# Kernel tuning notes

Measured on AMD Instinct MI355X. Metric: run time of the kernel, lower is better.

## Reference

```python
import jax, jax.numpy as jnp
import numpy as np

N_NODES = 100_000
N_EDGES = 1_000_000
IN_CH = 32
EDGE_CH = 16
OUT_CH = 32
D_CAT = 2 * IN_CH + EDGE_CH  # 80
D_MID = 56                   # linspace(80, 32, 3)[1]


def setup_inputs() -> dict:
    key = jax.random.key(0)
    ks = jax.random.split(key, 8)
    x = jax.random.normal(ks[0], (N_NODES, IN_CH), dtype=jnp.float32)
    edge_index = jax.random.randint(ks[1], (2, N_EDGES), 0, N_NODES, dtype=jnp.int64)
    edge_attr = jax.random.normal(ks[2], (N_EDGES, EDGE_CH), dtype=jnp.float32)
    # MLP params: Linear(80->56), Linear(56->32), bias=True (homogeneous_flag=False)
    W1 = jax.random.normal(ks[3], (D_CAT, D_MID), dtype=jnp.float32) / np.sqrt(D_CAT).astype(np.float32)
    b1 = jnp.zeros((D_MID,), dtype=jnp.float32)
    W2 = jax.random.normal(ks[4], (D_MID, OUT_CH), dtype=jnp.float32) / np.sqrt(D_MID).astype(np.float32)
    b2 = jnp.zeros((OUT_CH,), dtype=jnp.float32)
    return {"x": x, "edge_index": edge_index, "edge_attr": edge_attr,
            "W1": W1, "b1": b1, "W2": W2, "b2": b2}


def reference(x, edge_index, edge_attr, W1, b1, W2, b2):
    num_nodes = x.shape[0]
    rol, col = edge_index[0], edge_index[1]
    # gather node pairs + concat edge features: [E, 2*in + edge]
    e = jnp.concatenate([x[rol], x[col], edge_attr], axis=-1)
    # edge MLP (LeakyReLU after every layer, as in IterGNN's MLP)
    h = jax.nn.leaky_relu(e @ W1 + b1)
    v = jax.nn.leaky_relu(h @ W2 + b2)  # [E, out]
    # Max aggregation by destination node (scatter-max); empty segments -> 0
    agg = jax.ops.segment_max(v, col, num_segments=num_nodes)
    agg = jnp.where(jnp.isneginf(agg), jnp.zeros((), dtype=agg.dtype), agg)
    # elementwise max with trailing slice of input features
    out = jnp.maximum(agg, x[:, -v.shape[-1]:])
    return out
```

## Files before the change

### kernel.cpp

```cpp
#include <hip/hip_runtime.h>

#define N_NODES 100000
#define IN_CH 32
#define EDGE_CH 16
#define OUT_CH 32
#define D_CAT 80
#define D_MID 56

#define BKT_SHIFT 6
#define BKT_NODES 64
#define NB 1563
#define NB_ALL 1568
#define CAP 1024

#define NSUP 196
#define CAP_SUP 5632
#define K1_EDGES 4096
#define K2_ITERS 11

#define EPB 256
#define NT_E 16

#define W1F_SH 4096
#define W2F_SH 2048
#define W1D_SH 2048
#define WIMG_SH (W1F_SH + W2F_SH + W1D_SH)
#define FEATF_SH (NT_E * 2 * 64 * 8)

#define HSTRIDE 68
#define AGG_LD 33
#define ENC_NEGINF 0x007FFFFFu

typedef short short8 __attribute__((ext_vector_type(8)));
typedef float f32x4 __attribute__((ext_vector_type(4)));
typedef int i32x2 __attribute__((ext_vector_type(2)));

#define WS_IMG    0
#define WS_B1     16384
#define WS_B2     16640
#define WS_SUPCNT 16768
#define WS_GCNT   17664
#define WS_SUPREC 24576
#define WS_REC    8855552
#define WS_XB_A   21700608
#define XB_BYTES  6400000
#define WS_NEED_A ((size_t)WS_XB_A)
#define WS_NEED_AX ((size_t)WS_XB_A + XB_BYTES)
#define WS_XB_B   12869632
#define WS_NEED_B ((size_t)WS_XB_B)
#define WS_NEED_BX ((size_t)WS_XB_B + XB_BYTES)

__device__ __forceinline__ unsigned fenc(float f) {
    unsigned u = __float_as_uint(f);
    return (u & 0x80000000u) ? ~u : (u | 0x80000000u);
}
__device__ __forceinline__ float fdec(unsigned u) {
    u = (u & 0x80000000u) ? (u ^ 0x80000000u) : ~u;
    return __uint_as_float(u);
}
__device__ __forceinline__ float bfr(float f) {
    unsigned u = __float_as_uint(f);
    u = (u + 0x7FFFu + ((u >> 16) & 1u)) & 0xFFFF0000u;
    return __uint_as_float(u);
}
__device__ __forceinline__ unsigned short bf16b(float f) {
    unsigned u = __float_as_uint(f);
    return (unsigned short)((u + 0x7FFFu + ((u >> 16) & 1u)) >> 16);
}
__device__ __forceinline__ short8 cvt8(float4 a, float4 b) {
    return short8{ (short)bf16b(a.x), (short)bf16b(a.y), (short)bf16b(a.z), (short)bf16b(a.w),
                   (short)bf16b(b.x), (short)bf16b(b.y), (short)bf16b(b.z), (short)bf16b(b.w) };
}

__device__ __forceinline__ void convert_x_bf16(const float* __restrict__ x,
                                               unsigned short* __restrict__ xb,
                                               int gtid, int gstride) {
    const int tot = N_NODES * IN_CH / 8;
    for (int i = gtid; i < tot; i += gstride) {
        float4 a = ((const float4*)x)[2 * i];
        float4 b = ((const float4*)x)[2 * i + 1];
        *(short8*)&xb[i * 8] = cvt8(a, b);
    }
}

__device__ void build_weight_image(const float* __restrict__ W1, const float* __restrict__ b1,
                                   const float* __restrict__ W2, const float* __restrict__ b2,
                                   unsigned short* __restrict__ wsImg,
                                   float* __restrict__ wsb1, float* __restrict__ wsb2,
                                   int t, int nthr) {
    for (int s = t; s < W1F_SH; s += nthr) {
        int j = s & 7, l = (s >> 3) & 63, fi = s >> 9;
        int nt = fi & 3, ks = fi >> 2;
        int n = nt * 16 + (l & 15), kl = ks * 32 + (l >> 4) * 8 + j;
        unsigned short v = 0;
        if (n < D_MID) {
            if (kl < 32) v = bf16b(W1[kl * D_MID + n]);
            else if (kl < 48) v = bf16b(W1[(64 + kl - 32) * D_MID + n]);
        }
        wsImg[s] = v;
    }
    for (int s = t; s < W2F_SH; s += nthr) {
        int j = s & 7, l = (s >> 3) & 63, fi = s >> 9;
        int nt = fi & 1, ks = fi >> 1;
        int n = nt * 16 + (l & 15), kl = ks * 32 + (l >> 4) * 8 + j;
        wsImg[W1F_SH + s] = (kl < D_MID) ? bf16b(W2[kl * OUT_CH + n]) : (unsigned short)0;
    }
    for (int s = t; s < W1D_SH; s += nthr) {
        int j = s & 7, l = (s >> 3) & 63, fi = s >> 9;
        int nt = fi & 3;
        int n = nt * 16 + (l & 15), kl = (l >> 4) * 8 + j;
        wsImg[W1F_SH + W2F_SH + s] = (n < D_MID) ? bf16b(W1[(32 + kl) * D_MID + n]) : (unsigned short)0;
    }
    if (t < 64) wsb1[t] = (t < D_MID) ? bfr(b1[t]) : 0.f;
    else if (t < 96) wsb2[t - 64] = bfr(b2[t - 64]);
}

__global__ __launch_bounds__(512) void coarse_bin(
    const int* __restrict__ ei, int nE, int* __restrict__ gSupCnt, int2* __restrict__ supRec,
    const float* __restrict__ W1, const float* __restrict__ b1,
    const float* __restrict__ W2, const float* __restrict__ b2,
    unsigned short* __restrict__ wsImg, float* __restrict__ wsb1, float* __restrict__ wsb2)
{
    __shared__ int2 staged[K1_EDGES];
    __shared__ int cnt[256], sc[256], cur[256], wb[256];
    const int t = threadIdx.x;
    if (blockIdx.x == 0) build_weight_image(W1, b1, W2, b2, wsImg, wsb1, wsb2, t, 512);
    if (t < 256) cnt[t] = 0;
    __syncthreads();

    const int lo = blockIdx.x * K1_EDGES;
    int rdst[8], rsrc[8];
#pragma unroll
    for (int k = 0; k < 8; ++k) {
        int e = lo + k * 512 + t;
        bool v = e < nE;
        rdst[k] = v ? __builtin_nontemporal_load(ei + nE + e) : -1;
        rsrc[k] = v ? __builtin_nontemporal_load(ei + e) : 0;
        if ((unsigned)rdst[k] >= N_NODES) rdst[k] = -1;
        if ((unsigned)rsrc[k] >= N_NODES) rsrc[k] = 0;
        if (rdst[k] >= 0) atomicAdd(&cnt[rdst[k] >> 9], 1);
    }
    __syncthreads();
    if (t < 256) sc[t] = cnt[t];
    __syncthreads();
    for (int off = 1; off < 256; off <<= 1) {
        int v = 0;
        if (t < 256 && t >= off) v = sc[t - off];
        __syncthreads();
        if (t < 256) sc[t] += v;
        __syncthreads();
    }
    if (t < NSUP) {
        int c = cnt[t];
        int excl = sc[t] - c;
        int g = c ? atomicAdd(&gSupCnt[t], c) : 0;
        wb[t] = t * CAP_SUP + g - excl;
        cur[t] = excl;
    }
    __syncthreads();
#pragma unroll
    for (int k = 0; k < 8; ++k) {
        if (rdst[k] >= 0) {
            int s = rdst[k] >> 9;
            int pos = atomicAdd(&cur[s], 1);
            int e = lo + k * 512 + t;
            staged[pos] = make_int2(rsrc[k] | (s << 24), ((rdst[k] & 511) << 20) | e);
        }
    }
    __syncthreads();
    int nv = sc[NSUP - 1];
    for (int i = t; i < nv; i += 512) {
        int2 r = staged[i];
        int s = (unsigned)r.x >> 24;
        int addr = wb[s] + i;
        if (addr - s * CAP_SUP < CAP_SUP)
            supRec[addr] = make_int2(r.x & 0x00FFFFFF, r.y);
    }
}

__global__ __launch_bounds__(512) void fine_bin(
    const int* __restrict__ gSupCnt, const int2* __restrict__ supRec,
    int* __restrict__ gCnt, int2* __restrict__ rec,
    const float* __restrict__ x, unsigned short* __restrict__ xb)
{
    __shared__ int cur8[8];
    const int s = blockIdx.x, t = threadIdx.x;
    const int lane = t & 63;

    if (xb) convert_x_bf16(x, xb, s * 512 + t, NSUP * 512);

    const int cntS = min(gSupCnt[s], CAP_SUP);
    if (t < 8) cur8[t] = 0;
    __syncthreads();

    int2 r[K2_ITERS];
#pragma unroll
    for (int k = 0; k < K2_ITERS; ++k) {
        int i = k * 512 + t;
        r[k] = (i < cntS) ? supRec[(size_t)s * CAP_SUP + i] : make_int2(0, 0);
    }
#pragma unroll
    for (int k = 0; k < K2_ITERS; ++k) {
        int i = k * 512 + t;
        bool v = i < cntS;
        int f = v ? ((r[k].y >> 26) & 7) : -1;
        int rank = 0, wbase = 0;
#pragma unroll
        for (int vv = 0; vv < 8; ++vv) {
            unsigned long long m = __ballot(f == vv);
            if (lane == vv) wbase = m ? atomicAdd(&cur8[vv], (int)__popcll(m)) : 0;
            if (f == vv) rank = (int)__popcll(m & ((1ull << lane) - 1ull));
        }
        int base = __shfl(wbase, f & 7);
        if (v) {
            int pos = base + rank;
            if (pos < CAP)
                rec[(size_t)(s * 8 + f) * CAP + pos] =
                    make_int2(r[k].x, (((r[k].y >> 20) & 63) << 20) | (r[k].y & 0xFFFFF));
        }
    }
    __syncthreads();
    if (t < 8) gCnt[s * 8 + t] = min(cur8[t], CAP);
}

__global__ __launch_bounds__(512) void scatter_append(
    const int* __restrict__ ei, int* __restrict__ gCnt, int2* __restrict__ rec, int nE,
    const float* __restrict__ W1, const float* __restrict__ b1,
    const float* __restrict__ W2, const float* __restrict__ b2,
    unsigned short* __restrict__ wsImg, float* __restrict__ wsb1, float* __restrict__ wsb2,
    const float* __restrict__ x, unsigned short* __restrict__ xb)
{
    __shared__ int lh[NB];
    __shared__ int lbase[NB];
    if (blockIdx.x == 0) build_weight_image(W1, b1, W2, b2, wsImg, wsb1, wsb2, threadIdx.x, 512);
    if (xb) convert_x_bf16(x, xb, blockIdx.x * 512 + threadIdx.x, gridDim.x * 512);
    for (int i = threadIdx.x; i < NB; i += 512) lh[i] = 0;
    __syncthreads();
    int per = (nE + gridDim.x - 1) / gridDim.x;
    int lo = blockIdx.x * per;
    int hi = min(lo + per, nE);
    for (int e = lo + threadIdx.x; e < hi; e += 512) {
        int dst = __builtin_nontemporal_load(ei + nE + e);
        if ((unsigned)dst < N_NODES) atomicAdd(&lh[dst >> BKT_SHIFT], 1);
    }
    __syncthreads();
    for (int i = threadIdx.x; i < NB; i += 512) {
        int c = lh[i];
        lbase[i] = c ? atomicAdd(&gCnt[i], c) : 0;
        lh[i] = 0;
    }
    __syncthreads();
    for (int e = lo + threadIdx.x; e < hi; e += 512) {
        int dst = __builtin_nontemporal_load(ei + nE + e);
        if ((unsigned)dst >= N_NODES) continue;
        int b = dst >> BKT_SHIFT;
        int p = lbase[b] + atomicAdd(&lh[b], 1);
        if (p >= CAP) continue;
        int src = __builtin_nontemporal_load(ei + e);
        if ((unsigned)src >= N_NODES) src = 0;
        rec[(size_t)b * CAP + p] = make_int2(src, ((dst & (BKT_NODES - 1)) << 20) | e);
    }
}

template<int XB>
__global__ __launch_bounds__(512, 4) void bucket_mlp(
    const float* __restrict__ x, const unsigned short* __restrict__ xb,
    const float* __restrict__ ea,
    const int2* __restrict__ rec, const int* __restrict__ gCnt,
    const unsigned short* __restrict__ wsImg,
    const float* __restrict__ wsb1, const float* __restrict__ wsb2,
    float* __restrict__ out)
{
    __shared__ unsigned short sFeatF[FEATF_SH];
    __shared__ unsigned short sWgt[WIMG_SH];
    __shared__ float sHdst[BKT_NODES * HSTRIDE];
    __shared__ unsigned aggL[BKT_NODES * AGG_LD];
    __shared__ float sb1f[64];
    __shared__ float sb2f[32];
    __shared__ int sdl[EPB];

    unsigned short* const sW1F = sWgt;
    unsigned short* const sW2F = sWgt + W1F_SH;
    unsigned short* const sW1D = sWgt + W1F_SH + W2F_SH;
    unsigned short* const sHF  = sFeatF;

    const int t = threadIdx.x;
    const int nodeBase = blockIdx.x << BKT_SHIFT;
    const int base = blockIdx.x * CAP;
    const int cnt  = min(gCnt[blockIdx.x], CAP);

    for (int i = t; i < WIMG_SH / 8; i += 512)
        *(short8*)&sWgt[i * 8] = *(const short8*)(wsImg + i * 8);
    for (int i = t; i < BKT_NODES * AGG_LD; i += 512) aggL[i] = ENC_NEGINF;
    if (t < 64) sb1f[t] = wsb1[t];
    else if (t < 96) sb2f[t - 64] = wsb2[t - 64];

    const int wave = t >> 6;
    const int l15  = t & 15;
    const int quad = (t & 63) >> 4;
    const int lane = t & 63;
    const int slot = t >> 1, q = t & 1;
    const int sl15 = slot & 15, set = slot >> 4;

    short8 rv16[4];
    int rdl;

    auto loadRec = [&](int idx) -> i32x2 {
        return (idx < cnt) ? *(const i32x2*)(rec + base + idx) : (i32x2){0, 0};
    };
    auto gather = [&](i32x2 r2, bool ok) {
        rdl = ok ? ((r2.y >> 20) & 63) : -1;
        short8 z = {0, 0, 0, 0, 0, 0, 0, 0};
        if (q == 0) {
            if constexpr (XB) {
                const short8* xs8 = (const short8*)(xb + (size_t)r2.x * IN_CH);
#pragma unroll
                for (int k = 0; k < 4; ++k) rv16[k] = ok ? xs8[k] : z;
            } else {
                const float* xs = x + (size_t)r2.x * IN_CH;
#pragma unroll
                for (int k = 0; k < 4; ++k)
                    rv16[k] = ok ? cvt8(((const float4*)xs)[2 * k], ((const float4*)xs)[2 * k + 1]) : z;
            }
        } else {
            const float* ep = ea + (size_t)(r2.y & 0xFFFFF) * EDGE_CH;
#pragma unroll
            for (int k = 0; k < 2; ++k)
                rv16[k] = ok ? cvt8(((const float4*)ep)[2 * k], ((const float4*)ep)[2 * k + 1]) : z;
            rv16[2] = z; rv16[3] = z;
        }
    };
    auto storeChunk = [&]() {
        if (q == 0) sdl[slot] = rdl;
#pragma unroll
        for (int k = 0; k < 4; ++k) {
            int cj = q * 4 + k;
            int a16 = (set * 2 + (cj >> 2)) * 64 + (cj & 3) * 16 + sl15;
            *(short8*)&sFeatF[a16 * 8] = rv16[k];
        }
    };

    i32x2 recC = loadRec(slot);
    i32x2 recN = loadRec(EPB + slot);
    gather(recC, slot < cnt);

    __syncthreads();

    {
        const int ntile = wave & 3, mh = wave >> 2;
        int node = nodeBase + ntile * 16 + l15;
        short8 bfr8 = {0, 0, 0, 0, 0, 0, 0, 0};
        if (node < N_NODES) {
            if constexpr (XB) {
                bfr8 = *(const short8*)(xb + (size_t)node * IN_CH + quad * 8);
            } else {
                const float* xp = x + (size_t)node * IN_CH + quad * 8;
                bfr8 = cvt8(((const float4*)xp)[0], ((const float4*)xp)[1]);
            }
        }
        f32x4 accd[2] = {(f32x4){0.f, 0.f, 0.f, 0.f}, (f32x4){0.f, 0.f, 0.f, 0.f}};
#pragma unroll
        for (int i = 0; i < 2; ++i) {
            int nt = mh * 2 + i;
            short8 af = *(const short8*)&sW1D[(nt * 64 + lane) * 8];
            accd[i] = __builtin_amdgcn_mfma_f32_16x16x32_bf16(af, bfr8, accd[i], 0, 0, 0);
        }
#pragma unroll
        for (int i = 0; i < 2; ++i) {
            int nt = mh * 2 + i, c0 = nt * 16 + quad * 4;
            float4 vv;
#pragma unroll
            for (int j = 0; j < 4; ++j) {
                int c = c0 + j;
                ((float*)&vv)[j] = (c < D_MID) ? accd[i][j] + sb1f[c] : 0.f;
            }
            *(float4*)&sHdst[(ntile * 16 + l15) * HSTRIDE + c0] = vv;
        }
    }

    for (int c0e = 0; c0e < cnt; c0e += EPB) {
        storeChunk();
        __syncthreads();
        gather(recN, (c0e + EPB + slot) < cnt);
        recN = loadRec(c0e + 2 * EPB + slot);

        f32x4 acc[2][4];
#pragma unroll
        for (int ei = 0; ei < 2; ++ei)
#pragma unroll
            for (int nt = 0; nt < 4; ++nt) acc[ei][nt] = (f32x4){0.f, 0.f, 0.f, 0.f};
#pragma unroll
        for (int ks = 0; ks < 2; ++ks) {
            short8 bf0 = *(const short8*)&sFeatF[((wave * 2 + ks) * 64 + lane) * 8];
            short8 bf1 = *(const short8*)&sFeatF[(((wave + 8) * 2 + ks) * 64 + lane) * 8];
#pragma unroll
            for (int nt = 0; nt < 4; ++nt) {
                short8 af = *(const short8*)&sW1F[((ks * 4 + nt) * 64 + lane) * 8];
                acc[0][nt] = __builtin_amdgcn_mfma_f32_16x16x32_bf16(af, bf0, acc[0][nt], 0, 0, 0);
                acc[1][nt] = __builtin_amdgcn_mfma_f32_16x16x32_bf16(af, bf1, acc[1][nt], 0, 0, 0);
            }
        }
        __syncthreads();

#pragma unroll
        for (int ei = 0; ei < 2; ++ei) {
            int et = wave + ei * 8;
            int dl = sdl[et * 16 + l15];
            const float* hrow = &sHdst[((dl >= 0) ? dl : 0) * HSTRIDE];
#pragma unroll
            for (int nt = 0; nt < 4; ++nt) {
                int c0 = nt * 16 + quad * 4;
                float4 hd = *(const float4*)&hrow[c0];
                int ks2 = nt >> 1;
                int quad2 = (nt * 2 + (quad >> 1)) & 3;
                int off = (quad & 1) * 4;
                ushort4 p;
#pragma unroll
                for (int j = 0; j < 4; ++j) {
                    float v = acc[ei][nt][j] + ((const float*)&hd)[j];
                    v = (v > 0.f) ? v : 0.01f * v;
                    ((unsigned short*)&p)[j] = (c0 + j < D_MID) ? bf16b(v) : (unsigned short)0;
                }
                *(ushort4*)&sHF[((et * 2 + ks2) * 64 + quad2 * 16 + l15) * 8 + off] = p;
            }
        }
        __syncthreads();

        f32x4 acc2[2][2];
#pragma unroll
        for (int ei = 0; ei < 2; ++ei)
#pragma unroll
            for (int nt = 0; nt < 2; ++nt) acc2[ei][nt] = (f32x4){0.f, 0.f, 0.f, 0.f};
#pragma unroll
        for (int ks = 0; ks < 2; ++ks) {
            short8 bf0 = *(const short8*)&sHF[((wave * 2 + ks) * 64 + lane) * 8];
            short8 bf1 = *(const short8*)&sHF[(((wave + 8) * 2 + ks) * 64 + lane) * 8];
#pragma unroll
            for (int nt = 0; nt < 2; ++nt) {
                short8 af = *(const short8*)&sW2F[((ks * 2 + nt) * 64 + lane) * 8];
                acc2[0][nt] = __builtin_amdgcn_mfma_f32_16x16x32_bf16(af, bf0, acc2[0][nt], 0, 0, 0);
                acc2[1][nt] = __builtin_amdgcn_mfma_f32_16x16x32_bf16(af, bf1, acc2[1][nt], 0, 0, 0);
            }
        }

#pragma unroll
        for (int ei = 0; ei < 2; ++ei) {
            int et = wave + ei * 8;
            int dl = sdl[et * 16 + l15];
            if (dl >= 0) {
                unsigned* arow = &aggL[dl * AGG_LD];
#pragma unroll
                for (int nt = 0; nt < 2; ++nt) {
                    int c0 = nt * 16 + quad * 4;
#pragma unroll
                    for (int j = 0; j < 4; ++j) {
                        float v = acc2[ei][nt][j] + sb2f[c0 + j];
                        v = (v > 0.f) ? v : 0.01f * v;
                        atomicMax(arow + c0 + j, fenc(bfr(v)));
                    }
                }
            }
        }
        __syncthreads();
    }
    __syncthreads();

    {
        int nl = t >> 3, g4 = t & 7;
        int node = nodeBase + nl;
        if (node < N_NODES) {
            const unsigned* ar = &aggL[nl * AGG_LD + g4 * 4];
            float4 o;
            if constexpr (XB) {
                ushort4 xw = ((const ushort4*)(xb + (size_t)node * IN_CH))[g4];
                o.x = fmaxf((ar[0] == ENC_NEGINF) ? 0.f : fdec(ar[0]), __uint_as_float((unsigned)xw.x << 16));
                o.y = fmaxf((ar[1] == ENC_NEGINF) ? 0.f : fdec(ar[1]), __uint_as_float((unsigned)xw.y << 16));
                o.z = fmaxf((ar[2] == ENC_NEGINF) ? 0.f : fdec(ar[2]), __uint_as_float((unsigned)xw.z << 16));
                o.w = fmaxf((ar[3] == ENC_NEGINF) ? 0.f : fdec(ar[3]), __uint_as_float((unsigned)xw.w << 16));
            } else {
                float4 xv = ((const float4*)(x + (size_t)node * IN_CH))[g4];
                o.x = fmaxf((ar[0] == ENC_NEGINF) ? 0.f : fdec(ar[0]), bfr(xv.x));
                o.y = fmaxf((ar[1] == ENC_NEGINF) ? 0.f : fdec(ar[1]), bfr(xv.y));
                o.z = fmaxf((ar[2] == ENC_NEGINF) ? 0.f : fdec(ar[2]), bfr(xv.z));
                o.w = fmaxf((ar[3] == ENC_NEGINF) ? 0.f : fdec(ar[3]), bfr(xv.w));
            }
            ((float4*)(out + (size_t)node * OUT_CH))[g4] = o;
        }
    }
}

extern "C" void kernel_launch(void* const* d_in, const int* in_sizes, int n_in,
                              void* d_out, int out_size, void* d_ws, size_t ws_size,
                              hipStream_t stream) {
    const float* x  = (const float*)d_in[0];
    const int*   ei = (const int*)d_in[1];
    const float* ea = (const float*)d_in[2];
    const float* W1 = (const float*)d_in[3];
    const float* b1 = (const float*)d_in[4];
    const float* W2 = (const float*)d_in[5];
    const float* b2 = (const float*)d_in[6];

    char* ws = (char*)d_ws;
    unsigned short* wsImg = (unsigned short*)(ws + WS_IMG);
    float* wsb1 = (float*)(ws + WS_B1);
    float* wsb2 = (float*)(ws + WS_B2);
    int* gSupCnt = (int*)(ws + WS_SUPCNT);
    int* gCnt = (int*)(ws + WS_GCNT);

    const int nE = in_sizes[1] / 2;
    float* out = (float*)d_out;

    if (ws_size >= WS_NEED_A) {
        int2* supRec = (int2*)(ws + WS_SUPREC);
        int2* rec    = (int2*)(ws + WS_REC);
        bool xbOn = ws_size >= WS_NEED_AX;
        unsigned short* xb = xbOn ? (unsigned short*)(ws + WS_XB_A) : nullptr;
        hipMemsetAsync(gSupCnt, 0, NSUP * sizeof(int), stream);
        coarse_bin<<<(nE + K1_EDGES - 1) / K1_EDGES, 512, 0, stream>>>(
            ei, nE, gSupCnt, supRec, W1, b1, W2, b2, wsImg, wsb1, wsb2);
        fine_bin<<<NSUP, 512, 0, stream>>>(gSupCnt, supRec, gCnt, rec, x, xb);
        if (xbOn)
            bucket_mlp<1><<<NB, 512, 0, stream>>>(x, xb, ea, rec, gCnt, wsImg, wsb1, wsb2, out);
        else
            bucket_mlp<0><<<NB, 512, 0, stream>>>(x, nullptr, ea, rec, gCnt, wsImg, wsb1, wsb2, out);
    } else {
        int2* rec = (int2*)(ws + 24576);
        bool xbOn = ws_size >= WS_NEED_BX;
        unsigned short* xb = xbOn ? (unsigned short*)(ws + WS_XB_B) : nullptr;
        hipMemsetAsync(gCnt, 0, NB_ALL * sizeof(int), stream);
        scatter_append<<<128, 512, 0, stream>>>(ei, gCnt, rec, nE, W1, b1, W2, b2,
                                                wsImg, wsb1, wsb2, x, xb);
        if (xbOn)
            bucket_mlp<1><<<NB, 512, 0, stream>>>(x, xb, ea, rec, gCnt, wsImg, wsb1, wsb2, out);
        else
            bucket_mlp<0><<<NB, 512, 0, stream>>>(x, nullptr, ea, rec, gCnt, wsImg, wsb1, wsb2, out);
    }
}
```

Before: 208.5 us.

## Simplify coarse binning and split fine binning across blocks with global atomics

The coarse binning kernel drops its LDS staging buffer and block-wide prefix scan. Each edge record is now written straight to its super-bucket slot, using a global atomic base plus a local counter, and each block handles half as many edges. The fine binning kernel splits every super-bucket across four blocks that reserve bucket slots with global atomics on gCnt, which is now zeroed by a widened memset. The aim is more parallelism and fewer barriers in the preprocessing stages, at the cost of scattered uncoalesced writes, more global atomic traffic and gCnt no longer being clamped to CAP.

```diff
diff --git a/kernel.cpp b/kernel.cpp
--- a/kernel.cpp
+++ b/kernel.cpp
@@ -15,8 +15,11 @@
 
 #define NSUP 196
 #define CAP_SUP 5632
-#define K1_EDGES 4096
-#define K2_ITERS 11
+#define K1_EDGES 2048
+#define K1_EPT 4
+#define K2_SPLIT 4
+#define K2_SLICE 1408
+#define K2_SITERS 3
 
 #define EPB 256
 #define NT_E 16
@@ -40,6 +43,8 @@
 #define WS_B2     16640
 #define WS_SUPCNT 16768
 #define WS_GCNT   17664
+#define WS_Z0     16768
+#define WS_ZSZ    (17664 + 6272 - 16768)
 #define WS_SUPREC 24576
 #define WS_REC    8855552
 #define WS_XB_A   21700608
@@ -121,17 +126,16 @@
     const float* __restrict__ W2, const float* __restrict__ b2,
     unsigned short* __restrict__ wsImg, float* __restrict__ wsb1, float* __restrict__ wsb2)
 {
-    __shared__ int2 staged[K1_EDGES];
-    __shared__ int cnt[256], sc[256], cur[256], wb[256];
+    __shared__ int cnt[256], wb[256], cur[256];
     const int t = threadIdx.x;
     if (blockIdx.x == 0) build_weight_image(W1, b1, W2, b2, wsImg, wsb1, wsb2, t, 512);
     if (t < 256) cnt[t] = 0;
     __syncthreads();
 
     const int lo = blockIdx.x * K1_EDGES;
-    int rdst[8], rsrc[8];
-#pragma unroll
-    for (int k = 0; k < 8; ++k) {
+    int rdst[K1_EPT], rsrc[K1_EPT];
+#pragma unroll
+    for (int k = 0; k < K1_EPT; ++k) {
         int e = lo + k * 512 + t;
         bool v = e < nE;
         rdst[k] = v ? __builtin_nontemporal_load(ei + nE + e) : -1;
@@ -141,40 +145,23 @@
         if (rdst[k] >= 0) atomicAdd(&cnt[rdst[k] >> 9], 1);
     }
     __syncthreads();
-    if (t < 256) sc[t] = cnt[t];
-    __syncthreads();
-    for (int off = 1; off < 256; off <<= 1) {
-        int v = 0;
-        if (t < 256 && t >= off) v = sc[t - off];
-        __syncthreads();
-        if (t < 256) sc[t] += v;
-        __syncthreads();
-    }
-    if (t < NSUP) {
+    if (t < 256) {
         int c = cnt[t];
-        int excl = sc[t] - c;
-        int g = c ? atomicAdd(&gSupCnt[t], c) : 0;
-        wb[t] = t * CAP_SUP + g - excl;
-        cur[t] = excl;
-    }
-    __syncthreads();
-#pragma unroll
-    for (int k = 0; k < 8; ++k) {
+        wb[t] = c ? atomicAdd(&gSupCnt[t], c) : 0;
+        cur[t] = 0;
+    }
+    __syncthreads();
+#pragma unroll
+    for (int k = 0; k < K1_EPT; ++k) {
         if (rdst[k] >= 0) {
             int s = rdst[k] >> 9;
-            int pos = atomicAdd(&cur[s], 1);
-            int e = lo + k * 512 + t;
-            staged[pos] = make_int2(rsrc[k] | (s << 24), ((rdst[k] & 511) << 20) | e);
-        }
-    }
-    __syncthreads();
-    int nv = sc[NSUP - 1];
-    for (int i = t; i < nv; i += 512) {
-        int2 r = staged[i];
-        int s = (unsigned)r.x >> 24;
-        int addr = wb[s] + i;
-        if (addr - s * CAP_SUP < CAP_SUP)
-            supRec[addr] = make_int2(r.x & 0x00FFFFFF, r.y);
+            int pos = wb[s] + atomicAdd(&cur[s], 1);
+            if (pos < CAP_SUP) {
+                int e = lo + k * 512 + t;
+                supRec[(size_t)s * CAP_SUP + pos] =
+                    make_int2(rsrc[k], ((rdst[k] & 511) << 20) | e);
+            }
+        }
     }
 }
 
@@ -183,32 +170,32 @@
     int* __restrict__ gCnt, int2* __restrict__ rec,
     const float* __restrict__ x, unsigned short* __restrict__ xb)
 {
-    __shared__ int cur8[8];
-    const int s = blockIdx.x, t = threadIdx.x;
-    const int lane = t & 63;
-
-    if (xb) convert_x_bf16(x, xb, s * 512 + t, NSUP * 512);
+    const int blk = blockIdx.x;
+    const int s = blk >> 2, sl = blk & (K2_SPLIT - 1);
+    const int t = threadIdx.x, lane = t & 63;
+
+    if (xb) convert_x_bf16(x, xb, blk * 512 + t, NSUP * K2_SPLIT * 512);
 
     const int cntS = min(gSupCnt[s], CAP_SUP);
-    if (t < 8) cur8[t] = 0;
-    __syncthreads();
-
-    int2 r[K2_ITERS];
-#pragma unroll
-    for (int k = 0; k < K2_ITERS; ++k) {
-        int i = k * 512 + t;
-        r[k] = (i < cntS) ? supRec[(size_t)s * CAP_SUP + i] : make_int2(0, 0);
-    }
-#pragma unroll
-    for (int k = 0; k < K2_ITERS; ++k) {
-        int i = k * 512 + t;
-        bool v = i < cntS;
+    const int lo = sl * K2_SLICE;
+    const int hi = min(cntS, lo + K2_SLICE);
+
+    int2 r[K2_SITERS];
+#pragma unroll
+    for (int k = 0; k < K2_SITERS; ++k) {
+        int i = lo + k * 512 + t;
+        r[k] = (i < hi) ? supRec[(size_t)s * CAP_SUP + i] : make_int2(0, 0);
+    }
+#pragma unroll
+    for (int k = 0; k < K2_SITERS; ++k) {
+        int i = lo + k * 512 + t;
+        bool v = i < hi;
         int f = v ? ((r[k].y >> 26) & 7) : -1;
         int rank = 0, wbase = 0;
 #pragma unroll
         for (int vv = 0; vv < 8; ++vv) {
             unsigned long long m = __ballot(f == vv);
-            if (lane == vv) wbase = m ? atomicAdd(&cur8[vv], (int)__popcll(m)) : 0;
+            if (lane == vv) wbase = m ? atomicAdd(&gCnt[s * 8 + vv], (int)__popcll(m)) : 0;
             if (f == vv) rank = (int)__popcll(m & ((1ull << lane) - 1ull));
         }
         int base = __shfl(wbase, f & 7);
@@ -219,8 +206,6 @@
                     make_int2(r[k].x, (((r[k].y >> 20) & 63) << 20) | (r[k].y & 0xFFFFF));
         }
     }
-    __syncthreads();
-    if (t < 8) gCnt[s * 8 + t] = min(cur8[t], CAP);
 }
 
 __global__ __launch_bounds__(512) void scatter_append(
@@ -515,10 +500,10 @@
         int2* rec    = (int2*)(ws + WS_REC);
         bool xbOn = ws_size >= WS_NEED_AX;
         unsigned short* xb = xbOn ? (unsigned short*)(ws + WS_XB_A) : nullptr;
-        hipMemsetAsync(gSupCnt, 0, NSUP * sizeof(int), stream);
+        hipMemsetAsync(ws + WS_Z0, 0, WS_ZSZ, stream);
         coarse_bin<<<(nE + K1_EDGES - 1) / K1_EDGES, 512, 0, stream>>>(
             ei, nE, gSupCnt, supRec, W1, b1, W2, b2, wsImg, wsb1, wsb2);
-        fine_bin<<<NSUP, 512, 0, stream>>>(gSupCnt, supRec, gCnt, rec, x, xb);
+        fine_bin<<<NSUP * K2_SPLIT, 512, 0, stream>>>(gSupCnt, supRec, gCnt, rec, x, xb);
         if (xbOn)
             bucket_mlp<1><<<NB, 512, 0, stream>>>(x, xb, ea, rec, gCnt, wsImg, wsb1, wsb2, out);
         else
```

Measured after the change: 225.2 us. 8.0% more time.
